# Optimization experiments

Hardware: AMD Instinct MI355X
Metric: run time of the kernel (lower is better)

The kernel has to match this reference:

```python
import jax, jax.numpy as jnp
import numpy as np

B = 65536      # num_agents * num_processes
NUM = 16       # num_entities (landmarks tracked per agent)


def setup_inputs() -> dict:
    key = jax.random.key(0)
    k = jax.random.split(key, 6)
    value = jax.random.normal(k[0], (B, NUM * 2), jnp.float32)          # last abs positions
    vel = jax.random.normal(k[1], (B, NUM * 2), jnp.float32) * 0.1     # kalman velocities
    A = jax.random.normal(k[2], (B, NUM, 4, 4), jnp.float32) * 0.5
    P = A @ jnp.swapaxes(A, -1, -2) + jnp.eye(4, dtype=jnp.float32) * 0.1  # PSD covariances
    obs = jax.random.normal(k[3], (B, NUM * 2), jnp.float32)            # observed abs positions
    lm = jax.random.randint(k[4], (B, NUM), 0, 8, jnp.int32)            # last-mask age counters
    mask = jax.random.randint(k[5], (B, NUM), 0, 2, jnp.int32)          # current visibility
    return {"value": value, "vel": vel, "P": P, "obs": obs, "lm": lm, "mask": mask}


def _forward(value, vel, P, obs, lm, mask):
    Bn, two_num = value.shape
    num = two_num // 2
    # ---- _infer: constant-velocity predict (dt = 1). NOTE: original code builds Q
    # but never adds it to predicted_P, so we faithfully omit it too.
    Fm = jnp.array([[1., 0., 1., 0.],
                    [0., 1., 0., 1.],
                    [0., 0., 1., 0.],
                    [0., 0., 0., 1.]], jnp.float32)
    states = jnp.concatenate([value.reshape(Bn, num, 2), vel.reshape(Bn, num, 2)], axis=-1)  # [B,n,4]
    pred = jnp.einsum('ij,bnj->bni', Fm, states)                 # F @ state
    pP = jnp.einsum('ij,bnjk,lk->bnil', Fm, P, Fm)               # F P F^T  [B,n,4,4]
    lv = pred[..., :2]
    lvel = pred[..., 2:]
    obs2 = obs.reshape(Bn, num, 2)

    # ---- _merge_tensor: Kalman update with H = [[1,0,0,0],[0,1,0,0]], R = 1e-5 I
    R = jnp.float32(1e-5)
    S = pP[..., :2, :2] + R * jnp.eye(2, dtype=jnp.float32)      # [B,n,2,2]
    det = S[..., 0, 0] * S[..., 1, 1] - S[..., 0, 1] * S[..., 1, 0]
    Sinv = jnp.stack([jnp.stack([S[..., 1, 1], -S[..., 0, 1]], -1),
                      jnp.stack([-S[..., 1, 0], S[..., 0, 0]], -1)], -2) / det[..., None, None]
    K = jnp.einsum('bnij,bnjk->bnik', pP[..., :, :2], Sinv)      # P H^T S^-1  [B,n,4,2]
    y = obs2 - lv                                                # innovation
    upd = pred + jnp.einsum('bnij,bnj->bni', K, y)               # [B,n,4]
    Pn = pP - jnp.einsum('bnij,bnjk->bnik', K, pP[..., :2, :])   # (I - K H) P

    # ---- _fuse condition logic (faithful, including the original's rP bugs:
    # rP for cond2 and cond3b is never written -> stays zero)
    lmf = lm.astype(jnp.float32)
    mf = mask.astype(jnp.float32)
    c1 = (lmf == 0) & (mf == 0)
    c2 = (lmf == 0) & (mf != 0)
    c3 = (lmf != 0) & (mf == 0)
    c4 = (lmf != 0) & (mf != 0)
    c3a = c3 & (lmf <= 5)
    c3e, c4e, c3ae = c3[..., None], c4[..., None], c3a[..., None]
    rv = jnp.where(c4e, upd[..., :2], jnp.where(c3e, lv, obs2))
    rvel = jnp.where(c4e, upd[..., 2:], jnp.where(c3ae, lvel, 0.))
    rm = jnp.where(c2 | c4, 1., jnp.where(c3a, lmf + 1., 0.))
    diagP = jnp.diag(jnp.array([1., 1., 10., 10.], jnp.float32))
    rP = jnp.where(c1[..., None, None], diagP,
                   jnp.where(c3a[..., None, None], pP,
                             jnp.where(c4[..., None, None], Pn, 0.)))
    return rv.reshape(Bn, -1), rm, rvel.reshape(Bn, -1), rP


def reference(value, vel, P, obs, lm, mask):
    return _forward(value, vel, P, obs, lm, mask)
```

## Files before the change

### kernel.cpp

```cpp
#include <hip/hip_runtime.h>

#define NUM 16

__global__ __launch_bounds__(256) void kf_update_kernel(
    const float* __restrict__ value,
    const float* __restrict__ vel,
    const float* __restrict__ Pin,
    const float* __restrict__ obs,
    const int*   __restrict__ lm,
    const int*   __restrict__ mask,
    float* __restrict__ out,
    int Bn)
{
    const int tid = blockIdx.x * blockDim.x + threadIdx.x;
    const int total = Bn * NUM;
    if (tid >= total) return;

    const float2 v = reinterpret_cast<const float2*>(value)[tid];
    const float2 u = reinterpret_cast<const float2*>(vel)[tid];
    const float2 o = reinterpret_cast<const float2*>(obs)[tid];
    float Pm[16];
    {
        const float4* Pp = reinterpret_cast<const float4*>(Pin) + (size_t)tid * 4;
        float4 r0 = Pp[0], r1 = Pp[1], r2 = Pp[2], r3 = Pp[3];
        Pm[0]=r0.x; Pm[1]=r0.y; Pm[2]=r0.z; Pm[3]=r0.w;
        Pm[4]=r1.x; Pm[5]=r1.y; Pm[6]=r1.z; Pm[7]=r1.w;
        Pm[8]=r2.x; Pm[9]=r2.y; Pm[10]=r2.z; Pm[11]=r2.w;
        Pm[12]=r3.x; Pm[13]=r3.y; Pm[14]=r3.z; Pm[15]=r3.w;
    }
    const int l = lm[tid];
    const int m = mask[tid];

    const float p0 = v.x + u.x;
    const float p1 = v.y + u.y;
    const float p2 = u.x;
    const float p3 = u.y;

    float Q[4][4];
    #pragma unroll
    for (int j = 0; j < 4; ++j) {
        Q[0][j] = Pm[0*4+j] + Pm[2*4+j];
        Q[1][j] = Pm[1*4+j] + Pm[3*4+j];
        Q[2][j] = Pm[2*4+j];
        Q[3][j] = Pm[3*4+j];
    }
    float pP[4][4];
    #pragma unroll
    for (int i = 0; i < 4; ++i) {
        pP[i][0] = Q[i][0] + Q[i][2];
        pP[i][1] = Q[i][1] + Q[i][3];
        pP[i][2] = Q[i][2];
        pP[i][3] = Q[i][3];
    }

    const float S00 = pP[0][0] + 1e-5f;
    const float S01 = pP[0][1];
    const float S10 = pP[1][0];
    const float S11 = pP[1][1] + 1e-5f;
    const float det = S00 * S11 - S01 * S10;
    const float rdet = 1.0f / det;

    float K0[4], K1[4];
    #pragma unroll
    for (int i = 0; i < 4; ++i) {
        K0[i] = (pP[i][0] * S11 - pP[i][1] * S10) * rdet;
        K1[i] = (pP[i][1] * S00 - pP[i][0] * S01) * rdet;
    }

    const float y0 = o.x - p0;
    const float y1 = o.y - p1;
    const float upd0 = p0 + K0[0] * y0 + K1[0] * y1;
    const float upd1 = p1 + K0[1] * y0 + K1[1] * y1;
    const float upd2 = p2 + K0[2] * y0 + K1[2] * y1;
    const float upd3 = p3 + K0[3] * y0 + K1[3] * y1;

    float Pn[4][4];
    #pragma unroll
    for (int i = 0; i < 4; ++i) {
        #pragma unroll
        for (int j = 0; j < 4; ++j) {
            Pn[i][j] = pP[i][j] - (K0[i] * pP[0][j] + K1[i] * pP[1][j]);
        }
    }

    const bool c1  = (l == 0) && (m == 0);
    const bool c2  = (l == 0) && (m != 0);
    const bool c3  = (l != 0) && (m == 0);
    const bool c4  = (l != 0) && (m != 0);
    const bool c3a = c3 && (l <= 5);

    const float rv0  = c4 ? upd0 : (c3 ? p0 : o.x);
    const float rv1  = c4 ? upd1 : (c3 ? p1 : o.y);
    const float rvl0 = c4 ? upd2 : (c3a ? p2 : 0.0f);
    const float rvl1 = c4 ? upd3 : (c3a ? p3 : 0.0f);
    const float rmv  = (c2 || c4) ? 1.0f : (c3a ? (float)(l + 1) : 0.0f);

    float* rv_out   = out;
    float* rm_out   = out + (size_t)Bn * 32;
    float* rvel_out = out + (size_t)Bn * 48;
    float* rP_out   = out + (size_t)Bn * 80;

    reinterpret_cast<float2*>(rv_out)[tid]   = make_float2(rv0, rv1);
    rm_out[tid] = rmv;
    reinterpret_cast<float2*>(rvel_out)[tid] = make_float2(rvl0, rvl1);

    float4 w[4];
    #pragma unroll
    for (int i = 0; i < 4; ++i) {
        float e[4];
        #pragma unroll
        for (int j = 0; j < 4; ++j) {
            const float diag = (i == j) ? ((i < 2) ? 1.0f : 10.0f) : 0.0f;
            e[j] = c1 ? diag : (c3a ? pP[i][j] : (c4 ? Pn[i][j] : 0.0f));
        }
        w[i] = make_float4(e[0], e[1], e[2], e[3]);
    }
    float4* rPp = reinterpret_cast<float4*>(rP_out) + (size_t)tid * 4;
    rPp[0] = w[0]; rPp[1] = w[1]; rPp[2] = w[2]; rPp[3] = w[3];
}

extern "C" void kernel_launch(void* const* d_in, const int* in_sizes, int n_in,
                              void* d_out, int out_size, void* d_ws, size_t ws_size,
                              hipStream_t stream) {
    const float* value = (const float*)d_in[0];
    const float* vel   = (const float*)d_in[1];
    const float* P     = (const float*)d_in[2];
    const float* obs   = (const float*)d_in[3];
    const int*   lm    = (const int*)d_in[4];
    const int*   mask  = (const int*)d_in[5];

    const int Bn    = in_sizes[0] / (2 * NUM);
    const int total = Bn * NUM;

    kf_update_kernel<<<(total + 255) / 256, 256, 0, stream>>>(
        value, vel, P, obs, lm, mask, (float*)d_out, Bn);
}
```

Measured before the change: 181.1 us.

## Stage covariance loads and stores through padded shared memory for coalescing

The 4x4 covariance input and output go through a padded LDS tile. Each global float4 access is now fully coalesced across the block, where before each thread read and wrote a 64-byte strided chunk. This costs 20 KB of LDS per block, which may lower occupancy, plus extra barriers and LDS traffic. The kernel is memory-bound, so the goal is better DRAM transaction efficiency.

```diff
diff --git a/kernel.cpp b/kernel.cpp
--- a/kernel.cpp
+++ b/kernel.cpp
@@ -1,8 +1,10 @@
 #include <hip/hip_runtime.h>
 
 #define NUM 16
+#define TPB 256
+#define PSTRIDE 20
 
-__global__ __launch_bounds__(256) void kf_update_kernel(
+__global__ __launch_bounds__(TPB) void kf_update_kernel(
     const float* __restrict__ value,
     const float* __restrict__ vel,
     const float* __restrict__ Pin,
@@ -12,24 +14,47 @@
     float* __restrict__ out,
     int Bn)
 {
-    const int tid = blockIdx.x * blockDim.x + threadIdx.x;
+    __shared__ float sm[TPB * PSTRIDE];
+
+    const int tid   = threadIdx.x;
+    const int gtid  = blockIdx.x * TPB + tid;
     const int total = Bn * NUM;
-    if (tid >= total) return;
+    const long long blockBase = (long long)blockIdx.x * TPB;
+    const bool active = gtid < total;
 
-    const float2 v = reinterpret_cast<const float2*>(value)[tid];
-    const float2 u = reinterpret_cast<const float2*>(vel)[tid];
-    const float2 o = reinterpret_cast<const float2*>(obs)[tid];
+    {
+        const float4* Pg = reinterpret_cast<const float4*>(Pin) + blockBase * 4;
+        const long long limit = (long long)total * 4 - blockBase * 4;
+        #pragma unroll
+        for (int k = 0; k < 4; ++k) {
+            const int g = tid + TPB * k;
+            if (g < limit) {
+                const float4 x = Pg[g];
+                const int tr = g >> 2, part = g & 3;
+                *reinterpret_cast<float4*>(&sm[tr * PSTRIDE + part * 4]) = x;
+            }
+        }
+    }
+
+    float2 v = make_float2(0.f, 0.f), u = v, o = v;
+    int l = 0, m = 0;
+    if (active) {
+        v = reinterpret_cast<const float2*>(value)[gtid];
+        u = reinterpret_cast<const float2*>(vel)[gtid];
+        o = reinterpret_cast<const float2*>(obs)[gtid];
+        l = lm[gtid];
+        m = mask[gtid];
+    }
+
+    __syncthreads();
+
     float Pm[16];
-    {
-        const float4* Pp = reinterpret_cast<const float4*>(Pin) + (size_t)tid * 4;
-        float4 r0 = Pp[0], r1 = Pp[1], r2 = Pp[2], r3 = Pp[3];
-        Pm[0]=r0.x; Pm[1]=r0.y; Pm[2]=r0.z; Pm[3]=r0.w;
-        Pm[4]=r1.x; Pm[5]=r1.y; Pm[6]=r1.z; Pm[7]=r1.w;
-        Pm[8]=r2.x; Pm[9]=r2.y; Pm[10]=r2.z; Pm[11]=r2.w;
-        Pm[12]=r3.x; Pm[13]=r3.y; Pm[14]=r3.z; Pm[15]=r3.w;
+    #pragma unroll
+    for (int c = 0; c < 4; ++c) {
+        const float4 x = *reinterpret_cast<const float4*>(&sm[tid * PSTRIDE + c * 4]);
+        Pm[c * 4 + 0] = x.x; Pm[c * 4 + 1] = x.y;
+        Pm[c * 4 + 2] = x.z; Pm[c * 4 + 3] = x.w;
     }
-    const int l = lm[tid];
-    const int m = mask[tid];
 
     const float p0 = v.x + u.x;
     const float p1 = v.y + u.y;
@@ -39,10 +64,10 @@
     float Q[4][4];
     #pragma unroll
     for (int j = 0; j < 4; ++j) {
-        Q[0][j] = Pm[0*4+j] + Pm[2*4+j];
-        Q[1][j] = Pm[1*4+j] + Pm[3*4+j];
-        Q[2][j] = Pm[2*4+j];
-        Q[3][j] = Pm[3*4+j];
+        Q[0][j] = Pm[0 * 4 + j] + Pm[2 * 4 + j];
+        Q[1][j] = Pm[1 * 4 + j] + Pm[3 * 4 + j];
+        Q[2][j] = Pm[2 * 4 + j];
+        Q[3][j] = Pm[3 * 4 + j];
     }
     float pP[4][4];
     #pragma unroll
@@ -57,7 +82,7 @@
     const float S01 = pP[0][1];
     const float S10 = pP[1][0];
     const float S11 = pP[1][1] + 1e-5f;
-    const float det = S00 * S11 - S01 * S10;
+    const float det  = S00 * S11 - S01 * S10;
     const float rdet = 1.0f / det;
 
     float K0[4], K1[4];
@@ -100,11 +125,14 @@
     float* rvel_out = out + (size_t)Bn * 48;
     float* rP_out   = out + (size_t)Bn * 80;
 
-    reinterpret_cast<float2*>(rv_out)[tid]   = make_float2(rv0, rv1);
-    rm_out[tid] = rmv;
-    reinterpret_cast<float2*>(rvel_out)[tid] = make_float2(rvl0, rvl1);
+    if (active) {
+        reinterpret_cast<float2*>(rv_out)[gtid]   = make_float2(rv0, rv1);
+        rm_out[gtid] = rmv;
+        reinterpret_cast<float2*>(rvel_out)[gtid] = make_float2(rvl0, rvl1);
+    }
 
-    float4 w[4];
+    __syncthreads();
+
     #pragma unroll
     for (int i = 0; i < 4; ++i) {
         float e[4];
@@ -113,10 +141,24 @@
             const float diag = (i == j) ? ((i < 2) ? 1.0f : 10.0f) : 0.0f;
             e[j] = c1 ? diag : (c3a ? pP[i][j] : (c4 ? Pn[i][j] : 0.0f));
         }
-        w[i] = make_float4(e[0], e[1], e[2], e[3]);
+        *reinterpret_cast<float4*>(&sm[tid * PSTRIDE + i * 4]) =
+            make_float4(e[0], e[1], e[2], e[3]);
     }
-    float4* rPp = reinterpret_cast<float4*>(rP_out) + (size_t)tid * 4;
-    rPp[0] = w[0]; rPp[1] = w[1]; rPp[2] = w[2]; rPp[3] = w[3];
+
+    __syncthreads();
+
+    {
+        float4* rPg = reinterpret_cast<float4*>(rP_out) + blockBase * 4;
+        const long long limit = (long long)total * 4 - blockBase * 4;
+        #pragma unroll
+        for (int k = 0; k < 4; ++k) {
+            const int g = tid + TPB * k;
+            if (g < limit) {
+                const int tr = g >> 2, part = g & 3;
+                rPg[g] = *reinterpret_cast<const float4*>(&sm[tr * PSTRIDE + part * 4]);
+            }
+        }
+    }
 }
 
 extern "C" void kernel_launch(void* const* d_in, const int* in_sizes, int n_in,
@@ -131,7 +173,8 @@
 
     const int Bn    = in_sizes[0] / (2 * NUM);
     const int total = Bn * NUM;
+    const int blocks = (total + TPB - 1) / TPB;
 
-    kf_update_kernel<<<(total + 255) / 256, 256, 0, stream>>>(
+    kf_update_kernel<<<blocks, TPB, 0, stream>>>(
         value, vel, P, obs, lm, mask, (float*)d_out, Bn);
 }
```

New measurement: 177.4 us, median of 2. -2.1%, faster.

## Stage covariance loads through padded LDS with double-buffered multi-tile blocks

Applied to the files above, without the earlier changes.

Each block now handles four tiles of 256 tracks. The covariance matrices are loaded with fully coalesced float4 reads and transposed through padded shared memory, so each thread no longer makes a strided 64-byte per-thread read. The next tile's loads are prefetched into registers while the current tile is computed, which is meant to overlap memory latency with work. The cost is a 40 KB LDS footprint that limits occupancy, plus extra barriers. Stores to the output remain strided per thread.

```diff
diff --git a/kernel.cpp b/kernel.cpp
--- a/kernel.cpp
+++ b/kernel.cpp
@@ -1,8 +1,11 @@
 #include <hip/hip_runtime.h>
 
 #define NUM 16
+#define TPB 256
+#define TILES 4
+#define PSTRIDE 20
 
-__global__ __launch_bounds__(256) void kf_update_kernel(
+__global__ __launch_bounds__(TPB) void kf_update_kernel(
     const float* __restrict__ value,
     const float* __restrict__ vel,
     const float* __restrict__ Pin,
@@ -12,111 +15,164 @@
     float* __restrict__ out,
     int Bn)
 {
-    const int tid = blockIdx.x * blockDim.x + threadIdx.x;
+    __shared__ float sm[2][TPB * PSTRIDE];
+
+    const int tid   = threadIdx.x;
     const int total = Bn * NUM;
-    if (tid >= total) return;
-
-    const float2 v = reinterpret_cast<const float2*>(value)[tid];
-    const float2 u = reinterpret_cast<const float2*>(vel)[tid];
-    const float2 o = reinterpret_cast<const float2*>(obs)[tid];
-    float Pm[16];
-    {
-        const float4* Pp = reinterpret_cast<const float4*>(Pin) + (size_t)tid * 4;
-        float4 r0 = Pp[0], r1 = Pp[1], r2 = Pp[2], r3 = Pp[3];
-        Pm[0]=r0.x; Pm[1]=r0.y; Pm[2]=r0.z; Pm[3]=r0.w;
-        Pm[4]=r1.x; Pm[5]=r1.y; Pm[6]=r1.z; Pm[7]=r1.w;
-        Pm[8]=r2.x; Pm[9]=r2.y; Pm[10]=r2.z; Pm[11]=r2.w;
-        Pm[12]=r3.x; Pm[13]=r3.y; Pm[14]=r3.z; Pm[15]=r3.w;
-    }
-    const int l = lm[tid];
-    const int m = mask[tid];
-
-    const float p0 = v.x + u.x;
-    const float p1 = v.y + u.y;
-    const float p2 = u.x;
-    const float p3 = u.y;
-
-    float Q[4][4];
-    #pragma unroll
-    for (int j = 0; j < 4; ++j) {
-        Q[0][j] = Pm[0*4+j] + Pm[2*4+j];
-        Q[1][j] = Pm[1*4+j] + Pm[3*4+j];
-        Q[2][j] = Pm[2*4+j];
-        Q[3][j] = Pm[3*4+j];
-    }
-    float pP[4][4];
-    #pragma unroll
-    for (int i = 0; i < 4; ++i) {
-        pP[i][0] = Q[i][0] + Q[i][2];
-        pP[i][1] = Q[i][1] + Q[i][3];
-        pP[i][2] = Q[i][2];
-        pP[i][3] = Q[i][3];
-    }
-
-    const float S00 = pP[0][0] + 1e-5f;
-    const float S01 = pP[0][1];
-    const float S10 = pP[1][0];
-    const float S11 = pP[1][1] + 1e-5f;
-    const float det = S00 * S11 - S01 * S10;
-    const float rdet = 1.0f / det;
-
-    float K0[4], K1[4];
-    #pragma unroll
-    for (int i = 0; i < 4; ++i) {
-        K0[i] = (pP[i][0] * S11 - pP[i][1] * S10) * rdet;
-        K1[i] = (pP[i][1] * S00 - pP[i][0] * S01) * rdet;
-    }
-
-    const float y0 = o.x - p0;
-    const float y1 = o.y - p1;
-    const float upd0 = p0 + K0[0] * y0 + K1[0] * y1;
-    const float upd1 = p1 + K0[1] * y0 + K1[1] * y1;
-    const float upd2 = p2 + K0[2] * y0 + K1[2] * y1;
-    const float upd3 = p3 + K0[3] * y0 + K1[3] * y1;
-
-    float Pn[4][4];
-    #pragma unroll
-    for (int i = 0; i < 4; ++i) {
-        #pragma unroll
-        for (int j = 0; j < 4; ++j) {
-            Pn[i][j] = pP[i][j] - (K0[i] * pP[0][j] + K1[i] * pP[1][j]);
-        }
-    }
-
-    const bool c1  = (l == 0) && (m == 0);
-    const bool c2  = (l == 0) && (m != 0);
-    const bool c3  = (l != 0) && (m == 0);
-    const bool c4  = (l != 0) && (m != 0);
-    const bool c3a = c3 && (l <= 5);
-
-    const float rv0  = c4 ? upd0 : (c3 ? p0 : o.x);
-    const float rv1  = c4 ? upd1 : (c3 ? p1 : o.y);
-    const float rvl0 = c4 ? upd2 : (c3a ? p2 : 0.0f);
-    const float rvl1 = c4 ? upd3 : (c3a ? p3 : 0.0f);
-    const float rmv  = (c2 || c4) ? 1.0f : (c3a ? (float)(l + 1) : 0.0f);
+    const int tile0 = blockIdx.x * TILES;
 
     float* rv_out   = out;
     float* rm_out   = out + (size_t)Bn * 32;
     float* rvel_out = out + (size_t)Bn * 48;
     float* rP_out   = out + (size_t)Bn * 80;
 
-    reinterpret_cast<float2*>(rv_out)[tid]   = make_float2(rv0, rv1);
-    rm_out[tid] = rmv;
-    reinterpret_cast<float2*>(rvel_out)[tid] = make_float2(rvl0, rvl1);
+    float4 g[4];
+    float2 pv = make_float2(0.f,0.f), pu = pv, po = pv;
+    int    pl = 0, pm_ = 0;
 
-    float4 w[4];
+    {
+        const long long base = (long long)tile0 * TPB;
+        const long long lim4 = (long long)total * 4 - base * 4;
+        const float4* Pg = reinterpret_cast<const float4*>(Pin) + base * 4;
+        #pragma unroll
+        for (int k = 0; k < 4; ++k)
+            g[k] = (tid + TPB * k < lim4) ? Pg[tid + TPB * k]
+                                          : make_float4(0.f,0.f,0.f,0.f);
+        const long long t = base + tid;
+        if (t < total) {
+            pv  = reinterpret_cast<const float2*>(value)[t];
+            pu  = reinterpret_cast<const float2*>(vel)[t];
+            po  = reinterpret_cast<const float2*>(obs)[t];
+            pl  = lm[t];
+            pm_ = mask[t];
+        }
+    }
     #pragma unroll
-    for (int i = 0; i < 4; ++i) {
-        float e[4];
+    for (int k = 0; k < 4; ++k) {
+        const int gi = tid + TPB * k, tr = gi >> 2, part = gi & 3;
+        *reinterpret_cast<float4*>(&sm[0][tr * PSTRIDE + part * 4]) = g[k];
+    }
+    __syncthreads();
+
+    for (int it = 0; it < TILES; ++it) {
+        const int cur = it & 1, nxt = cur ^ 1;
+        const long long base  = (long long)(tile0 + it) * TPB;
+        const long long track = base + tid;
+        const bool active = track < total;
+
+        const float2 v = pv, u = pu, o = po;
+        const int l = pl, m = pm_;
+
+        const bool havenext = (it + 1 < TILES) &&
+                              ((long long)(tile0 + it + 1) * TPB < total);
+        if (havenext) {
+            const long long nb   = (long long)(tile0 + it + 1) * TPB;
+            const long long lim4 = (long long)total * 4 - nb * 4;
+            const float4* Pg = reinterpret_cast<const float4*>(Pin) + nb * 4;
+            #pragma unroll
+            for (int k = 0; k < 4; ++k)
+                g[k] = (tid + TPB * k < lim4) ? Pg[tid + TPB * k]
+                                              : make_float4(0.f,0.f,0.f,0.f);
+            const long long nt = nb + tid;
+            if (nt < total) {
+                pv  = reinterpret_cast<const float2*>(value)[nt];
+                pu  = reinterpret_cast<const float2*>(vel)[nt];
+                po  = reinterpret_cast<const float2*>(obs)[nt];
+                pl  = lm[nt];
+                pm_ = mask[nt];
+            }
+        }
+
+        float Pm[16];
+        #pragma unroll
+        for (int c = 0; c < 4; ++c) {
+            const float4 x = *reinterpret_cast<const float4*>(
+                &sm[cur][tid * PSTRIDE + c * 4]);
+            Pm[c*4+0] = x.x; Pm[c*4+1] = x.y; Pm[c*4+2] = x.z; Pm[c*4+3] = x.w;
+        }
+
+        const float p0 = v.x + u.x;
+        const float p1 = v.y + u.y;
+        const float p2 = u.x;
+        const float p3 = u.y;
+
+        float Q[4][4];
         #pragma unroll
         for (int j = 0; j < 4; ++j) {
-            const float diag = (i == j) ? ((i < 2) ? 1.0f : 10.0f) : 0.0f;
-            e[j] = c1 ? diag : (c3a ? pP[i][j] : (c4 ? Pn[i][j] : 0.0f));
+            Q[0][j] = Pm[0*4+j] + Pm[2*4+j];
+            Q[1][j] = Pm[1*4+j] + Pm[3*4+j];
+            Q[2][j] = Pm[2*4+j];
+            Q[3][j] = Pm[3*4+j];
         }
-        w[i] = make_float4(e[0], e[1], e[2], e[3]);
+        float pP[4][4];
+        #pragma unroll
+        for (int i = 0; i < 4; ++i) {
+            pP[i][0] = Q[i][0] + Q[i][2];
+            pP[i][1] = Q[i][1] + Q[i][3];
+            pP[i][2] = Q[i][2];
+            pP[i][3] = Q[i][3];
+        }
+
+        const float S00 = pP[0][0] + 1e-5f;
+        const float S01 = pP[0][1];
+        const float S10 = pP[1][0];
+        const float S11 = pP[1][1] + 1e-5f;
+        const float rdet = 1.0f / (S00 * S11 - S01 * S10);
+
+        float K0[4], K1[4];
+        #pragma unroll
+        for (int i = 0; i < 4; ++i) {
+            K0[i] = (pP[i][0] * S11 - pP[i][1] * S10) * rdet;
+            K1[i] = (pP[i][1] * S00 - pP[i][0] * S01) * rdet;
+        }
+
+        const float y0 = o.x - p0;
+        const float y1 = o.y - p1;
+        const float upd0 = p0 + K0[0]*y0 + K1[0]*y1;
+        const float upd1 = p1 + K0[1]*y0 + K1[1]*y1;
+        const float upd2 = p2 + K0[2]*y0 + K1[2]*y1;
+        const float upd3 = p3 + K0[3]*y0 + K1[3]*y1;
+
+        const bool c1  = (l == 0) && (m == 0);
+        const bool c2  = (l == 0) && (m != 0);
+        const bool c3  = (l != 0) && (m == 0);
+        const bool c4  = (l != 0) && (m != 0);
+        const bool c3a = c3 && (l <= 5);
+
+        const float rv0  = c4 ? upd0 : (c3 ? p0 : o.x);
+        const float rv1  = c4 ? upd1 : (c3 ? p1 : o.y);
+        const float rvl0 = c4 ? upd2 : (c3a ? p2 : 0.0f);
+        const float rvl1 = c4 ? upd3 : (c3a ? p3 : 0.0f);
+        const float rmv  = (c2 || c4) ? 1.0f : (c3a ? (float)(l + 1) : 0.0f);
+
+        if (active) {
+            reinterpret_cast<float2*>(rv_out)[track]   = make_float2(rv0, rv1);
+            rm_out[track] = rmv;
+            reinterpret_cast<float2*>(rvel_out)[track] = make_float2(rvl0, rvl1);
+
+            float4* rPg = reinterpret_cast<float4*>(rP_out) + track * 4;
+            #pragma unroll
+            for (int i = 0; i < 4; ++i) {
+                float e[4];
+                #pragma unroll
+                for (int j = 0; j < 4; ++j) {
+                    const float Pn   = pP[i][j] - (K0[i]*pP[0][j] + K1[i]*pP[1][j]);
+                    const float diag = (i == j) ? ((i < 2) ? 1.0f : 10.0f) : 0.0f;
+                    e[j] = c1 ? diag : (c3a ? pP[i][j] : (c4 ? Pn : 0.0f));
+                }
+                rPg[i] = make_float4(e[0], e[1], e[2], e[3]);
+            }
+        }
+
+        if (havenext) {
+            #pragma unroll
+            for (int k = 0; k < 4; ++k) {
+                const int gi = tid + TPB * k, tr = gi >> 2, part = gi & 3;
+                *reinterpret_cast<float4*>(&sm[nxt][tr * PSTRIDE + part * 4]) = g[k];
+            }
+            __syncthreads();
+        }
     }
-    float4* rPp = reinterpret_cast<float4*>(rP_out) + (size_t)tid * 4;
-    rPp[0] = w[0]; rPp[1] = w[1]; rPp[2] = w[2]; rPp[3] = w[3];
 }
 
 extern "C" void kernel_launch(void* const* d_in, const int* in_sizes, int n_in,
@@ -131,7 +187,8 @@
 
     const int Bn    = in_sizes[0] / (2 * NUM);
     const int total = Bn * NUM;
+    const int blocks = (total + TPB * TILES - 1) / (TPB * TILES);
 
-    kf_update_kernel<<<(total + 255) / 256, 256, 0, stream>>>(
+    kf_update_kernel<<<blocks, TPB, 0, stream>>>(
         value, vel, P, obs, lm, mask, (float*)d_out, Bn);
 }
```

Result: no change. 180.7 us (-0.3%).
